# Optimization experiments

Hardware: AMD Instinct MI355X
Metric: run time of the kernel (lower is better)

## Reference

```python
import jax, jax.numpy as jnp
import numpy as np

B, N, FEAT, HID = 1024, 128, 512, 256


def setup_inputs() -> dict:
    key = jax.random.key(0)
    k1, k2, k3, k4, k5, k6 = jax.random.split(key, 6)
    x = jax.random.normal(k1, (B, FEAT), dtype=jnp.float32)
    labels = jax.random.randint(k2, (B,), 0, N, dtype=jnp.int64)
    W_proj = jax.random.normal(k3, (FEAT, HID), dtype=jnp.float32) / np.sqrt(FEAT)
    b_proj = jax.random.normal(k4, (HID,), dtype=jnp.float32) * 0.01
    means = jax.random.normal(k5, (N, HID), dtype=jnp.float32)
    # inverse covariances must be SPD so sqrt(dist_sq) is real
    A = jax.random.normal(k6, (N, HID, HID), dtype=jnp.float32)
    inv_covs = jnp.einsum('nij,nkj->nik', A, A) / HID + 0.1 * jnp.eye(HID, dtype=jnp.float32)
    return {"x": x, "labels": labels, "W_proj": W_proj, "b_proj": b_proj,
            "means": means, "inv_covs": inv_covs}


def reference(x, labels, W_proj, b_proj, means, inv_covs):
    b = x.shape[0]
    n = means.shape[0]
    x_proj = x @ W_proj + b_proj                       # (b, hid)
    delta = x_proj[:, None, :] - means[None, :, :]     # (b, n, hid)
    # batched Mahalanobis quadratic form
    dist_sq = jnp.einsum('bni,nij,bnj->bn', delta, inv_covs, delta)
    distmat = jnp.sqrt(dist_sq + 1e-12)                # (b, n)
    center_mask = (labels[:, None] == jnp.arange(n)[None, :]).astype(distmat.dtype)
    loss = jnp.clip(distmat * center_mask, 1e-12, 1e12).sum() / b
    return loss, distmat
```

## Files before the change

### kernel.cpp

```cpp
#include <hip/hip_runtime.h>
#include <hip/hip_bf16.h>

#define B_    1024
#define N_    128
#define FEAT_ 512
#define HID_  256

typedef __bf16 bf16x8 __attribute__((ext_vector_type(8)));
typedef float  f32x4  __attribute__((ext_vector_type(4)));

__device__ __forceinline__ unsigned int f2bf(float f) {
    unsigned int u = __float_as_uint(f);
    u += 0x7fffu + ((u >> 16) & 1u);
    return u >> 16;
}
__device__ __forceinline__ unsigned int pack2(float a, float b) {
    return f2bf(a) | (f2bf(b) << 16);
}

__global__ __launch_bounds__(256) void prep_kernel(
    const float* __restrict__ x, const float* __restrict__ W,
    const float* __restrict__ bias, const float* __restrict__ means,
    const float* __restrict__ invcov,
    float* __restrict__ xp, unsigned short* __restrict__ xbf,
    unsigned short* __restrict__ Mbf, float* __restrict__ v2,
    float* __restrict__ cpart)
{
    const int t = threadIdx.x;
    if (blockIdx.x < 256) {
        __shared__ float xs[4][FEAT_];
        const int b0 = blockIdx.x * 4;
        {
            const float4* xsrc = (const float4*)(x + (size_t)b0 * FEAT_);
            const float4 v0 = xsrc[t];
            const float4 v1 = xsrc[t + 256];
            ((float4*)&xs[0][0])[t]       = v0;
            ((float4*)&xs[0][0])[t + 256] = v1;
        }
        __syncthreads();
        const int h = t;
        const float bb = bias[h];
        float a0 = bb, a1 = bb, a2 = bb, a3 = bb;
        #pragma unroll 8
        for (int f = 0; f < FEAT_; ++f) {
            const float w = W[(size_t)f * HID_ + h];
            a0 += xs[0][f] * w;
            a1 += xs[1][f] * w;
            a2 += xs[2][f] * w;
            a3 += xs[3][f] * w;
        }
        xp [(size_t)(b0 + 0) * HID_ + h] = a0;
        xp [(size_t)(b0 + 1) * HID_ + h] = a1;
        xp [(size_t)(b0 + 2) * HID_ + h] = a2;
        xp [(size_t)(b0 + 3) * HID_ + h] = a3;
        xbf[(size_t)(b0 + 0) * HID_ + h] = (unsigned short)f2bf(a0);
        xbf[(size_t)(b0 + 1) * HID_ + h] = (unsigned short)f2bf(a1);
        xbf[(size_t)(b0 + 2) * HID_ + h] = (unsigned short)f2bf(a2);
        xbf[(size_t)(b0 + 3) * HID_ + h] = (unsigned short)f2bf(a3);
    } else {
        __shared__ float sv[16][33];
        __shared__ float sw[2];
        const int cb = blockIdx.x - 256;
        const int n  = cb >> 4;
        const int jg = cb & 15;
        const float* Mn = invcov + (size_t)n * (HID_ * HID_) + (size_t)jg * 16 * HID_;
        const float* mu = means + (size_t)n * HID_;
        unsigned short* Mb = Mbf + (size_t)n * (HID_ * HID_) + (size_t)jg * 16 * HID_;
        const int gc = t & 31;
        const int r0 = t >> 5;
        const float4 mk0 = *(const float4*)(mu + gc * 8);
        const float4 mk1 = *(const float4*)(mu + gc * 8 + 4);
        #pragma unroll
        for (int i = 0; i < 2; ++i) {
            const int row = r0 + i * 8;
            const float* src = Mn + (size_t)row * HID_ + gc * 8;
            const float4 a = *(const float4*)src;
            const float4 b = *(const float4*)(src + 4);
            const int g2 = gc ^ ((row & 7) << 2);
            *(uint4*)(Mb + (size_t)row * HID_ + g2 * 8) =
                make_uint4(pack2(a.x, a.y), pack2(a.z, a.w), pack2(b.x, b.y), pack2(b.z, b.w));
            sv[row][gc] = a.x * mk0.x + a.y * mk0.y + a.z * mk0.z + a.w * mk0.w
                        + b.x * mk1.x + b.y * mk1.y + b.z * mk1.z + b.w * mk1.w;
        }
        __syncthreads();
        if (t < 128) {
            const int row = t >> 3;
            const int i0  = (t & 7) * 4;
            float v = sv[row][i0] + sv[row][i0 + 1] + sv[row][i0 + 2] + sv[row][i0 + 3];
            v += __shfl_xor(v, 1);
            v += __shfl_xor(v, 2);
            v += __shfl_xor(v, 4);
            const int j = jg * 16 + row;
            if ((t & 7) == 0) v2[(size_t)n * HID_ + j] = 2.f * v;
            float cc = ((t & 7) == 0) ? v * mu[j] : 0.f;
            cc += __shfl_xor(cc, 8);
            cc += __shfl_xor(cc, 16);
            cc += __shfl_xor(cc, 32);
            if ((t & 63) == 0) sw[t >> 6] = cc;
        }
        __syncthreads();
        if (t == 0) cpart[cb] = sw[0] + sw[1];
    }
}

__global__ __launch_bounds__(512, 4) void dist_kernel(
    const float* __restrict__ xp, const unsigned short* __restrict__ xbf,
    const unsigned short* __restrict__ Mbf, const float* __restrict__ v2,
    float* __restrict__ p)
{
    extern __shared__ unsigned short Ms[];

    const int tid  = threadIdx.x;
    const int bh   = blockIdx.x;
    const int jh   = blockIdx.y;
    const int n    = blockIdx.z;
    const int wave = tid >> 6;
    const int lane = tid & 63;
    const int q    = lane >> 4;
    const int l    = lane & 15;

    const unsigned short* src = Mbf + (size_t)n * (HID_ * HID_) + (size_t)jh * 32768;
    #pragma unroll
    for (int i = 0; i < 8; ++i) {
        const int c = i * 8 + wave;
        __builtin_amdgcn_global_load_lds(
            (const __attribute__((address_space(1))) unsigned int*)(src + (size_t)c * 512 + lane * 8),
            (__attribute__((address_space(3))) unsigned int*)&Ms[c * 512],
            16, 0, 0);
    }

    bf16x8 afrag[2][8];
    #pragma unroll
    for (int rb = 0; rb < 2; ++rb) {
        const unsigned short* xr = xbf + (size_t)(bh * 256 + wave * 32 + rb * 16 + l) * HID_;
        #pragma unroll
        for (int kk = 0; kk < 8; ++kk)
            afrag[rb][kk] = *(const bf16x8*)(xr + kk * 32 + q * 8);
    }
    float v2l[8];
    #pragma unroll
    for (int ct = 0; ct < 8; ++ct)
        v2l[ct] = v2[(size_t)n * HID_ + jh * 128 + ct * 16 + l];

    __syncthreads();

    float part[8];
    #pragma unroll
    for (int i = 0; i < 8; ++i) part[i] = 0.f;

    const size_t xbase = (size_t)(bh * 256 + wave * 32 + q * 4) * HID_ + jh * 128 + l;

    #pragma unroll
    for (int ct = 0; ct < 8; ++ct) {
        float xl[8];
        #pragma unroll
        for (int rb = 0; rb < 2; ++rb)
            #pragma unroll
            for (int r = 0; r < 4; ++r)
                xl[rb * 4 + r] = xp[xbase + (size_t)(rb * 16 + r) * HID_ + ct * 16];

        f32x4 acc0 = {0.f,0.f,0.f,0.f}, acc1 = {0.f,0.f,0.f,0.f};
        #pragma unroll
        for (int kk = 0; kk < 8; ++kk) {
            const bf16x8 bfrag = *(const bf16x8*)&Ms[(ct * 16 + l) * HID_ +
                                                     (((kk * 4 + q) ^ ((l & 7) << 2)) << 3)];
            acc0 = __builtin_amdgcn_mfma_f32_16x16x32_bf16(afrag[0][kk], bfrag, acc0, 0, 0, 0);
            acc1 = __builtin_amdgcn_mfma_f32_16x16x32_bf16(afrag[1][kk], bfrag, acc1, 0, 0, 0);
        }
        const float vv = v2l[ct];
        #pragma unroll
        for (int r = 0; r < 4; ++r) {
            part[r]     += (acc0[r] - vv) * xl[r];
            part[4 + r] += (acc1[r] - vv) * xl[4 + r];
        }
    }

    #pragma unroll
    for (int i = 0; i < 8; ++i) {
        float v = part[i];
        v += __shfl_xor(v, 1);
        v += __shfl_xor(v, 2);
        v += __shfl_xor(v, 4);
        v += __shfl_xor(v, 8);
        part[i] = v;
    }
    if (l == 0) {
        float* pb = p + (size_t)jh * (B_ * N_);
        #pragma unroll
        for (int i = 0; i < 8; ++i) {
            const int row = bh * 256 + wave * 32 + (i >> 2) * 16 + q * 4 + (i & 3);
            pb[(size_t)row * N_ + n] = part[i];
        }
    }
}

__global__ __launch_bounds__(256) void finalize_kernel(
    const float* __restrict__ p, const float* __restrict__ cpart,
    float* __restrict__ out)
{
    __shared__ float sc[128];
    const int t = threadIdx.x;
    if (t < 128) {
        float s = 0.f;
        #pragma unroll
        for (int g = 0; g < 16; ++g) s += cpart[t * 16 + g];
        sc[t] = s;
    }
    __syncthreads();
    const int i = blockIdx.x * 256 + t;
    const int n = i & (N_ - 1);
    out[1 + i] = sqrtf(p[i] + p[B_ * N_ + i] + sc[n] + 1e-12f);
}

__global__ __launch_bounds__(1024) void loss_kernel(
    const float* __restrict__ distmat, const int* __restrict__ labels,
    float* __restrict__ out)
{
    __shared__ float red[16];
    const int b = threadIdx.x;
    float s = distmat[(size_t)b * N_ + labels[b]];
    #pragma unroll
    for (int m = 1; m <= 32; m <<= 1) s += __shfl_xor(s, m);
    if ((b & 63) == 0) red[b >> 6] = s;
    __syncthreads();
    if (b == 0) {
        float t = 0.f;
        #pragma unroll
        for (int i = 0; i < 16; ++i) t += red[i];
        out[0] = t / (float)B_ + (float)(N_ - 1) * 1e-12f;
    }
}

extern "C" void kernel_launch(void* const* d_in, const int* in_sizes, int n_in,
                              void* d_out, int out_size, void* d_ws, size_t ws_size,
                              hipStream_t stream) {
    const float* x      = (const float*)d_in[0];
    const int*   labels = (const int*)d_in[1];
    const float* W      = (const float*)d_in[2];
    const float* bias   = (const float*)d_in[3];
    const float* means  = (const float*)d_in[4];
    const float* invcov = (const float*)d_in[5];
    float* out = (float*)d_out;

    char* ws = (char*)d_ws;
    unsigned short* Mbf   = (unsigned short*)(ws);
    float*          xp    = (float*)         (ws + 16777216);
    unsigned short* xbf   = (unsigned short*)(ws + 17825792);
    float*          v2    = (float*)         (ws + 18350080);
    float*          cpart = (float*)         (ws + 18481152);
    float*          p     = (float*)         (ws + 18489344);

    constexpr int DIST_LDS = 128 * HID_ * 2;
    (void)hipFuncSetAttribute((const void*)dist_kernel,
                              hipFuncAttributeMaxDynamicSharedMemorySize, DIST_LDS);

    prep_kernel<<<dim3(2304), 256, 0, stream>>>(x, W, bias, means, invcov,
                                                xp, xbf, Mbf, v2, cpart);
    dist_kernel<<<dim3(4, 2, N_), 512, DIST_LDS, stream>>>(xp, xbf, Mbf, v2, p);
    finalize_kernel<<<dim3((B_ * N_) / 256), 256, 0, stream>>>(p, cpart, out);
    loss_kernel<<<1, 1024, 0, stream>>>(out + 1, labels, out);
}
```

Before: 146.5 us.

## Fold loss reduction into finalize kernel and drop LDS staging in projection

Removes the separate single-block loss kernel. The finalize kernel now computes each label-matched distance contribution, reduces it per wavefront and atomically adds it to the loss, which prep_kernel initialises with the epsilon term. The projection path now reads x directly from global memory as float4 instead of staging it in shared memory, dropping a barrier. The inverse-covariance conversion loop is manually unrolled so all four loads issue up front. This saves one launch and a serial reduction, at the cost of float atomics, which make the summation order nondeterministic.

```diff
diff --git a/kernel.cpp b/kernel.cpp
--- a/kernel.cpp
+++ b/kernel.cpp
@@ -24,30 +24,30 @@
     const float* __restrict__ invcov,
     float* __restrict__ xp, unsigned short* __restrict__ xbf,
     unsigned short* __restrict__ Mbf, float* __restrict__ v2,
-    float* __restrict__ cpart)
+    float* __restrict__ cpart, float* __restrict__ out)
 {
     const int t = threadIdx.x;
     if (blockIdx.x < 256) {
-        __shared__ float xs[4][FEAT_];
+        if (blockIdx.x == 0 && t == 0) out[0] = (float)(N_ - 1) * 1e-12f;
         const int b0 = blockIdx.x * 4;
-        {
-            const float4* xsrc = (const float4*)(x + (size_t)b0 * FEAT_);
-            const float4 v0 = xsrc[t];
-            const float4 v1 = xsrc[t + 256];
-            ((float4*)&xs[0][0])[t]       = v0;
-            ((float4*)&xs[0][0])[t + 256] = v1;
-        }
-        __syncthreads();
-        const int h = t;
+        const int h  = t;
         const float bb = bias[h];
         float a0 = bb, a1 = bb, a2 = bb, a3 = bb;
+        const float* xr = x + (size_t)b0 * FEAT_;
         #pragma unroll 8
-        for (int f = 0; f < FEAT_; ++f) {
-            const float w = W[(size_t)f * HID_ + h];
-            a0 += xs[0][f] * w;
-            a1 += xs[1][f] * w;
-            a2 += xs[2][f] * w;
-            a3 += xs[3][f] * w;
+        for (int f = 0; f < FEAT_; f += 4) {
+            const float4 xv0 = *(const float4*)(xr + 0 * FEAT_ + f);
+            const float4 xv1 = *(const float4*)(xr + 1 * FEAT_ + f);
+            const float4 xv2 = *(const float4*)(xr + 2 * FEAT_ + f);
+            const float4 xv3 = *(const float4*)(xr + 3 * FEAT_ + f);
+            const float w0 = W[(size_t)(f + 0) * HID_ + h];
+            const float w1 = W[(size_t)(f + 1) * HID_ + h];
+            const float w2 = W[(size_t)(f + 2) * HID_ + h];
+            const float w3 = W[(size_t)(f + 3) * HID_ + h];
+            a0 += xv0.x * w0 + xv0.y * w1 + xv0.z * w2 + xv0.w * w3;
+            a1 += xv1.x * w0 + xv1.y * w1 + xv1.z * w2 + xv1.w * w3;
+            a2 += xv2.x * w0 + xv2.y * w1 + xv2.z * w2 + xv2.w * w3;
+            a3 += xv3.x * w0 + xv3.y * w1 + xv3.z * w2 + xv3.w * w3;
         }
         xp [(size_t)(b0 + 0) * HID_ + h] = a0;
         xp [(size_t)(b0 + 1) * HID_ + h] = a1;
@@ -68,20 +68,24 @@
         unsigned short* Mb = Mbf + (size_t)n * (HID_ * HID_) + (size_t)jg * 16 * HID_;
         const int gc = t & 31;
         const int r0 = t >> 5;
+        const float* s0 = Mn + (size_t)r0 * HID_ + gc * 8;
+        const float* s1 = Mn + (size_t)(r0 + 8) * HID_ + gc * 8;
+        const float4 a0 = *(const float4*)s0;
+        const float4 b0 = *(const float4*)(s0 + 4);
+        const float4 a1 = *(const float4*)s1;
+        const float4 b1 = *(const float4*)(s1 + 4);
         const float4 mk0 = *(const float4*)(mu + gc * 8);
         const float4 mk1 = *(const float4*)(mu + gc * 8 + 4);
-        #pragma unroll
-        for (int i = 0; i < 2; ++i) {
-            const int row = r0 + i * 8;
-            const float* src = Mn + (size_t)row * HID_ + gc * 8;
-            const float4 a = *(const float4*)src;
-            const float4 b = *(const float4*)(src + 4);
-            const int g2 = gc ^ ((row & 7) << 2);
-            *(uint4*)(Mb + (size_t)row * HID_ + g2 * 8) =
-                make_uint4(pack2(a.x, a.y), pack2(a.z, a.w), pack2(b.x, b.y), pack2(b.z, b.w));
-            sv[row][gc] = a.x * mk0.x + a.y * mk0.y + a.z * mk0.z + a.w * mk0.w
-                        + b.x * mk1.x + b.y * mk1.y + b.z * mk1.z + b.w * mk1.w;
-        }
+        const int g20 = gc ^ ((r0 & 7) << 2);
+        const int g21 = gc ^ (((r0 + 8) & 7) << 2);
+        *(uint4*)(Mb + (size_t)r0 * HID_ + g20 * 8) =
+            make_uint4(pack2(a0.x, a0.y), pack2(a0.z, a0.w), pack2(b0.x, b0.y), pack2(b0.z, b0.w));
+        *(uint4*)(Mb + (size_t)(r0 + 8) * HID_ + g21 * 8) =
+            make_uint4(pack2(a1.x, a1.y), pack2(a1.z, a1.w), pack2(b1.x, b1.y), pack2(b1.z, b1.w));
+        sv[r0][gc]     = a0.x * mk0.x + a0.y * mk0.y + a0.z * mk0.z + a0.w * mk0.w
+                       + b0.x * mk1.x + b0.y * mk1.y + b0.z * mk1.z + b0.w * mk1.w;
+        sv[r0 + 8][gc] = a1.x * mk0.x + a1.y * mk0.y + a1.z * mk0.z + a1.w * mk0.w
+                       + b1.x * mk1.x + b1.y * mk1.y + b1.z * mk1.z + b1.w * mk1.w;
         __syncthreads();
         if (t < 128) {
             const int row = t >> 3;
@@ -196,7 +200,7 @@
 
 __global__ __launch_bounds__(256) void finalize_kernel(
     const float* __restrict__ p, const float* __restrict__ cpart,
-    float* __restrict__ out)
+    const int* __restrict__ labels, float* __restrict__ out)
 {
     __shared__ float sc[128];
     const int t = threadIdx.x;
@@ -209,26 +213,17 @@
     __syncthreads();
     const int i = blockIdx.x * 256 + t;
     const int n = i & (N_ - 1);
-    out[1 + i] = sqrtf(p[i] + p[B_ * N_ + i] + sc[n] + 1e-12f);
-}
-
-__global__ __launch_bounds__(1024) void loss_kernel(
-    const float* __restrict__ distmat, const int* __restrict__ labels,
-    float* __restrict__ out)
-{
-    __shared__ float red[16];
-    const int b = threadIdx.x;
-    float s = distmat[(size_t)b * N_ + labels[b]];
-    #pragma unroll
-    for (int m = 1; m <= 32; m <<= 1) s += __shfl_xor(s, m);
-    if ((b & 63) == 0) red[b >> 6] = s;
-    __syncthreads();
-    if (b == 0) {
-        float t = 0.f;
-        #pragma unroll
-        for (int i = 0; i < 16; ++i) t += red[i];
-        out[0] = t / (float)B_ + (float)(N_ - 1) * 1e-12f;
-    }
+    const int b = i >> 7;
+    const float d = sqrtf(p[i] + p[B_ * N_ + i] + sc[n] + 1e-12f);
+    out[1 + i] = d;
+    float c = (labels[b] == n) ? d * (1.f / (float)B_) : 0.f;
+    c += __shfl_xor(c, 1);
+    c += __shfl_xor(c, 2);
+    c += __shfl_xor(c, 4);
+    c += __shfl_xor(c, 8);
+    c += __shfl_xor(c, 16);
+    c += __shfl_xor(c, 32);
+    if ((t & 63) == 0 && c != 0.f) atomicAdd(out, c);
 }
 
 extern "C" void kernel_launch(void* const* d_in, const int* in_sizes, int n_in,
@@ -255,8 +250,7 @@
                               hipFuncAttributeMaxDynamicSharedMemorySize, DIST_LDS);
 
     prep_kernel<<<dim3(2304), 256, 0, stream>>>(x, W, bias, means, invcov,
-                                                xp, xbf, Mbf, v2, cpart);
+                                                xp, xbf, Mbf, v2, cpart, out);
     dist_kernel<<<dim3(4, 2, N_), 512, DIST_LDS, stream>>>(xp, xbf, Mbf, v2, p);
-    finalize_kernel<<<dim3((B_ * N_) / 256), 256, 0, stream>>>(p, cpart, out);
-    loss_kernel<<<1, 1024, 0, stream>>>(out + 1, labels, out);
-}
+    finalize_kernel<<<dim3((B_ * N_) / 256), 256, 0, stream>>>(p, cpart, labels, out);
+}
```

New measurement: 163.3 us. +11.5%, slower.
